# Performance work log

Measured on AMD Instinct MI355X. Metric: run time of the kernel, lower is better.

## Reference

```python
import jax, jax.numpy as jnp
import numpy as np

EPS = 1e-8  # F.cosine_similarity default eps


def setup_inputs() -> dict:
    key = jax.random.key(0)
    k1, = jax.random.split(key, 1)
    x = jax.random.normal(k1, (16384, 512), dtype=jnp.float32)
    w = jnp.float32(10.0)   # init_w parameter
    b = jnp.float32(-5.0)   # init_b parameter
    return {"x": x, "w": w, "b": b}


def reference(x, w, b):
    # x: [2N, D] interleaved (anchor, positive) embeddings
    anchor = x[0::2]    # [N, D]
    positive = x[1::2]  # [N, D]
    N = anchor.shape[0]

    # cosine similarity matrix: cos[i, j] = <pos_i, anc_j> / max(|pos_i||anc_j|, eps)
    # (normalize + GEMM instead of the O(N*D*N) broadcast)
    dots = jnp.einsum('id,jd->ij', positive, anchor)          # [N, N]
    pn = jnp.linalg.norm(positive, axis=1)                    # [N]
    an = jnp.linalg.norm(anchor, axis=1)                      # [N]
    denom = jnp.maximum(pn[:, None] * an[None, :], EPS)
    cos_sim = dots / denom

    logits = cos_sim * w + b                                  # [N, N]
    labels = jnp.arange(N)

    # CrossEntropyLoss (mean reduction)
    logp = jax.nn.log_softmax(logits, axis=1)
    nloss = -jnp.mean(logp[jnp.arange(N), labels])
    return nloss
```

## Files before the change

kernel.cpp:

```cpp
#include <hip/hip_runtime.h>
#include <hip/hip_bf16.h>

typedef __attribute__((ext_vector_type(8))) short short8;
typedef __attribute__((ext_vector_type(4))) float f32x4;

#define D 512
#define BM 64
#define BN 64
#define BK 64

__device__ inline unsigned pack2f(float lo, float hi) {
    __hip_bfloat162 v = __float22bfloat162_rn(make_float2(lo, hi));
    union { __hip_bfloat162 h; unsigned u; } cv;
    cv.h = v;
    return cv.u;
}

__device__ inline int4 pack8f(const float4& v0, const float4& v1, float sc) {
    int4 r;
    r.x = (int)pack2f(v0.x * sc, v0.y * sc);
    r.y = (int)pack2f(v0.z * sc, v0.w * sc);
    r.z = (int)pack2f(v1.x * sc, v1.y * sc);
    r.w = (int)pack2f(v1.z * sc, v1.w * sc);
    return r;
}

__global__ __launch_bounds__(256) void norm_kernel(
    const float* __restrict__ x,
    float* __restrict__ pinv, float* __restrict__ ainv,
    float* __restrict__ diag, float* __restrict__ sumexp,
    __hip_bfloat16* __restrict__ Pn, __hip_bfloat16* __restrict__ An, int cached)
{
    const int i = blockIdx.x, t = threadIdx.x;
    const float2* ap = (const float2*)(x + (size_t)(2 * i) * D);
    const float2* pp = (const float2*)(x + (size_t)(2 * i + 1) * D);
    float2 a = ap[t], p = pp[t];
    float ssa = a.x * a.x + a.y * a.y;
    float ssp = p.x * p.x + p.y * p.y;
    float dt  = p.x * a.x + p.y * a.y;
#pragma unroll
    for (int m = 1; m < 64; m <<= 1) {
        ssa += __shfl_xor(ssa, m);
        ssp += __shfl_xor(ssp, m);
        dt  += __shfl_xor(dt, m);
    }
    __shared__ float red[3][4];
    if ((t & 63) == 0) { int wv = t >> 6; red[0][wv] = ssa; red[1][wv] = ssp; red[2][wv] = dt; }
    __syncthreads();
    ssa = red[0][0] + red[0][1] + red[0][2] + red[0][3];
    ssp = red[1][0] + red[1][1] + red[1][2] + red[1][3];
    dt  = red[2][0] + red[2][1] + red[2][2] + red[2][3];
    float an = sqrtf(ssa), pn = sqrtf(ssp);
    float ia = 1.0f / fmaxf(an, 1e-30f);
    float ip = 1.0f / fmaxf(pn, 1e-30f);
    if (t == 0) {
        ainv[i] = ia;
        pinv[i] = ip;
        diag[i] = dt / fmaxf(pn * an, 1e-8f);
        sumexp[i] = 0.0f;
    }
    if (cached) {
        ((__hip_bfloat162*)(Pn + (size_t)i * D))[t] = __float22bfloat162_rn(make_float2(p.x * ip, p.y * ip));
        ((__hip_bfloat162*)(An + (size_t)i * D))[t] = __float22bfloat162_rn(make_float2(a.x * ia, a.y * ia));
    }
}

template<bool CACHED>
__global__ __launch_bounds__(256, 2) void gemm_lse_kernel(
    const float* __restrict__ x,
    const __hip_bfloat16* __restrict__ Pn, const __hip_bfloat16* __restrict__ An,
    const float* __restrict__ pinv, const float* __restrict__ ainv,
    const float* __restrict__ wp, float* __restrict__ sumexp, int N)
{
    __shared__ __align__(16) unsigned char lds[81920];
    unsigned char* As = lds;
    unsigned char* Bs = lds + 65536;

    const int t = threadIdx.x;
    const int rb = blockIdx.y, cs = blockIdx.x;
    const int lane = t & 63, w = t >> 6;
    const int wr = w >> 1, wc = w & 1;
    const int l15 = lane & 15, lhi = lane >> 4;

    const int colsPer = N >> 3;
    const int CT = colsPer / BN;
    const int Q = CT * (D / BK);

    {
        int r = t >> 2;
        int kq = (t & 3) << 7;
        int grow = rb * BM + r;
        if (CACHED) {
            const int4* src = (const int4*)(Pn + (size_t)grow * D);
#pragma unroll
            for (int i2 = 0; i2 < 16; ++i2) {
                int k0 = kq + i2 * 8;
                int4 v = src[k0 >> 3];
                *(int4*)(As + r * 1024 + ((k0 * 2) ^ ((r & 7) << 4))) = v;
            }
        } else {
            const float4* src = (const float4*)(x + (size_t)(2 * grow + 1) * D);
            float sc = pinv[grow];
#pragma unroll
            for (int i2 = 0; i2 < 16; ++i2) {
                int k0 = kq + i2 * 8;
                float4 v0 = src[k0 >> 2], v1 = src[(k0 >> 2) + 1];
                *(int4*)(As + r * 1024 + ((k0 * 2) ^ ((r & 7) << 4))) = pack8f(v0, v1, sc);
            }
        }
    }

    const int cl = t >> 2;
    const int kq = (t & 3) << 4;

    auto loadB = [&](int q, int4& oa, int4& ob) {
        int ct = q >> 3, kc = q & 7;
        int c = cs * colsPer + ct * BN + cl;
        int k = kc * BK + kq;
        if (CACHED) {
            const int4* src = (const int4*)(An + (size_t)c * D + k);
            oa = src[0]; ob = src[1];
        } else {
            const float4* src = (const float4*)(x + (size_t)(2 * c) * D + k);
            float sc = ainv[c];
            float4 v0 = src[0], v1 = src[1], v2 = src[2], v3 = src[3];
            oa = pack8f(v0, v1, sc);
            ob = pack8f(v2, v3, sc);
        }
    };
    auto writeB = [&](int buf, const int4& oa, const int4& ob) {
        unsigned char* bb = Bs + buf * 8192 + cl * 128;
        int kb0 = kq * 2;
        *(int4*)(bb + (kb0 ^ ((cl & 7) << 4))) = oa;
        *(int4*)(bb + ((kb0 + 16) ^ ((cl & 7) << 4))) = ob;
    };

    const float wv = *wp;
    const float s = fabsf(wv);

    int4 ba, bb2;
    loadB(0, ba, bb2);
    __syncthreads();
    writeB(0, ba, bb2);
    __syncthreads();

    f32x4 acc[2][2];
    float rs[2][4];
#pragma unroll
    for (int mi = 0; mi < 2; ++mi) {
#pragma unroll
        for (int j = 0; j < 4; ++j) rs[mi][j] = 0.0f;
#pragma unroll
        for (int ni = 0; ni < 2; ++ni) {
#pragma unroll
            for (int j = 0; j < 4; ++j) acc[mi][ni][j] = 0.0f;
        }
    }

    for (int q = 0; q < Q; ++q) {
        const int kc = q & 7;
        const bool more = (q + 1 < Q);
        if (more) loadB(q + 1, ba, bb2);
        const unsigned char* Bp = Bs + (q & 1) * 8192;
#pragma unroll
        for (int ks = 0; ks < 2; ++ks) {
            int ka = kc * 64 + ks * 32 + lhi * 8;
            int ra0 = wr * 32 + l15, ra1 = ra0 + 16;
            short8 a0 = *(const short8*)(As + ra0 * 1024 + ((ka * 2) ^ ((ra0 & 7) << 4)));
            short8 a1 = *(const short8*)(As + ra1 * 1024 + ((ka * 2) ^ ((ra1 & 7) << 4)));
            int kb = ks * 32 + lhi * 8;
            int c0 = wc * 32 + l15, c1 = c0 + 16;
            short8 b0 = *(const short8*)(Bp + c0 * 128 + ((kb * 2) ^ ((c0 & 7) << 4)));
            short8 b1 = *(const short8*)(Bp + c1 * 128 + ((kb * 2) ^ ((c1 & 7) << 4)));
            acc[0][0] = __builtin_amdgcn_mfma_f32_16x16x32_bf16(a0, b0, acc[0][0], 0, 0, 0);
            acc[0][1] = __builtin_amdgcn_mfma_f32_16x16x32_bf16(a0, b1, acc[0][1], 0, 0, 0);
            acc[1][0] = __builtin_amdgcn_mfma_f32_16x16x32_bf16(a1, b0, acc[1][0], 0, 0, 0);
            acc[1][1] = __builtin_amdgcn_mfma_f32_16x16x32_bf16(a1, b1, acc[1][1], 0, 0, 0);
        }
        if (kc == 7) {
#pragma unroll
            for (int mi = 0; mi < 2; ++mi) {
#pragma unroll
                for (int ni = 0; ni < 2; ++ni) {
#pragma unroll
                    for (int j = 0; j < 4; ++j) {
                        rs[mi][j] += __expf(acc[mi][ni][j] * wv - s);
                        acc[mi][ni][j] = 0.0f;
                    }
                }
            }
        }
        if (more) {
            __syncthreads();
            writeB((q + 1) & 1, ba, bb2);
            __syncthreads();
        }
    }

#pragma unroll
    for (int mi = 0; mi < 2; ++mi) {
#pragma unroll
        for (int j = 0; j < 4; ++j) {
            float v = rs[mi][j];
            v += __shfl_xor(v, 1);
            v += __shfl_xor(v, 2);
            v += __shfl_xor(v, 4);
            v += __shfl_xor(v, 8);
            if (l15 == 0) {
                int row = rb * BM + wr * 32 + mi * 16 + lhi * 4 + j;
                atomicAdd(&sumexp[row], v);
            }
        }
    }
}

__global__ __launch_bounds__(256) void finalize_kernel(
    const float* __restrict__ sumexp, const float* __restrict__ diag,
    const float* __restrict__ wp, float* __restrict__ out, int N)
{
    const int t = threadIdx.x;
    const float w = *wp;
    const float s = fabsf(w);
    float acc = 0.0f;
    for (int i = t; i < N; i += 256)
        acc += s + logf(sumexp[i]) - w * diag[i];
#pragma unroll
    for (int m = 1; m < 64; m <<= 1) acc += __shfl_xor(acc, m);
    __shared__ float red[4];
    if ((t & 63) == 0) red[t >> 6] = acc;
    __syncthreads();
    if (t == 0) out[0] = (red[0] + red[1] + red[2] + red[3]) / (float)N;
}

extern "C" void kernel_launch(void* const* d_in, const int* in_sizes, int n_in,
                              void* d_out, int out_size, void* d_ws, size_t ws_size,
                              hipStream_t stream) {
    const float* x  = (const float*)d_in[0];
    const float* wp = (const float*)d_in[1];

    const int N = in_sizes[0] / (2 * D);

    char* ws = (char*)d_ws;
    size_t nf = (size_t)N * 4;
    float* pinv   = (float*)(ws);
    float* ainv   = (float*)(ws + nf);
    float* diag   = (float*)(ws + 2 * nf);
    float* sumexp = (float*)(ws + 3 * nf);
    size_t base = (4 * nf + 255) & ~(size_t)255;
    __hip_bfloat16* Pn = (__hip_bfloat16*)(ws + base);
    __hip_bfloat16* An = (__hip_bfloat16*)(ws + base + (size_t)N * D * 2);
    const bool cached = ws_size >= base + (size_t)N * D * 4;

    norm_kernel<<<N, 256, 0, stream>>>(x, pinv, ainv, diag, sumexp, Pn, An, cached ? 1 : 0);

    dim3 grid(8, N / BM);
    if (cached)
        gemm_lse_kernel<true><<<grid, 256, 0, stream>>>(x, Pn, An, pinv, ainv, wp, sumexp, N);
    else
        gemm_lse_kernel<false><<<grid, 256, 0, stream>>>(x, Pn, An, pinv, ainv, wp, sumexp, N);

    finalize_kernel<<<1, 256, 0, stream>>>(sumexp, diag, wp, (float*)d_out, N);
}
```

Measured before the change: 218.5 us.

## Use 128x128 output tiles with direct global-to-LDS loads in cached GEMM path

Adds a new cached-path GEMM+LSE kernel that computes a full 128x128 output tile per block over a 2D grid. Each warp now holds 4x4 MFMA accumulators, and operands are streamed straight into LDS with global_load_lds. This replaces the old design, where a 64-row A panel stayed resident and each block swept a column slice. The aim is more MFMA work per LDS read and less per-tile load overhead. In exchange the tile loop is not double-buffered (load, sync, compute, sync), and atomics on sumexp increase because there are many column blocks. The finalize kernel is widened to 1024 threads.

```diff
diff --git a/kernel.cpp b/kernel.cpp
--- a/kernel.cpp
+++ b/kernel.cpp
@@ -5,9 +5,12 @@
 typedef __attribute__((ext_vector_type(4))) float f32x4;
 
 #define D 512
-#define BM 64
-#define BN 64
+#define BM 128
+#define BN 128
 #define BK 64
+
+typedef const __attribute__((address_space(1))) void gvoid;
+typedef __attribute__((address_space(3))) void lvoid;
 
 __device__ inline unsigned pack2f(float lo, float hi) {
     __hip_bfloat162 v = __float22bfloat162_rn(make_float2(lo, hi));
@@ -65,10 +68,92 @@
     }
 }
 
-template<bool CACHED>
-__global__ __launch_bounds__(256, 2) void gemm_lse_kernel(
+__global__ __launch_bounds__(256) void gemm_lse_128(
+    const __hip_bfloat16* __restrict__ Pn, const __hip_bfloat16* __restrict__ An,
+    const float* __restrict__ wp, float* __restrict__ sumexp)
+{
+    __shared__ __align__(16) unsigned char lds[32768];
+    unsigned char* As = lds;
+    unsigned char* Bs = lds + 16384;
+
+    const int t = threadIdx.x;
+    const int lane = t & 63, w = t >> 6;
+    const int wr = w >> 1, wc = w & 1;
+    const int l15 = lane & 15, lhi = lane >> 4;
+    const int brow = blockIdx.y * BM;
+    const int bcol = blockIdx.x * BN;
+
+    const float wv = *wp;
+    const float s = fabsf(wv);
+
+    f32x4 acc[4][4];
+#pragma unroll
+    for (int mi = 0; mi < 4; ++mi)
+#pragma unroll
+        for (int ni = 0; ni < 4; ++ni)
+#pragma unroll
+            for (int j = 0; j < 4; ++j) acc[mi][ni][j] = 0.0f;
+
+    const int o0 = t * 16;
+
+    for (int kt = 0; kt < D / BK; ++kt) {
+#pragma unroll
+        for (int i = 0; i < 4; ++i) {
+            int o = i * 4096 + o0;
+            int row = o >> 7;
+            int sslot = ((o >> 4) & 7) ^ (row & 7);
+            const __hip_bfloat16* ga = Pn + (size_t)(brow + row) * D + kt * BK + sslot * 8;
+            const __hip_bfloat16* gb = An + (size_t)(bcol + row) * D + kt * BK + sslot * 8;
+            __builtin_amdgcn_global_load_lds((gvoid*)ga, (lvoid*)(As + o), 16, 0, 0);
+            __builtin_amdgcn_global_load_lds((gvoid*)gb, (lvoid*)(Bs + o), 16, 0, 0);
+        }
+        __syncthreads();
+
+#pragma unroll
+        for (int ks = 0; ks < 2; ++ks) {
+            short8 a[4], b[4];
+            const int kb = ks * 64 + lhi * 16;
+#pragma unroll
+            for (int mi = 0; mi < 4; ++mi) {
+                int r = wr * 64 + mi * 16 + l15;
+                a[mi] = *(const short8*)(As + r * 128 + (kb ^ ((r & 7) << 4)));
+            }
+#pragma unroll
+            for (int ni = 0; ni < 4; ++ni) {
+                int c = wc * 64 + ni * 16 + l15;
+                b[ni] = *(const short8*)(Bs + c * 128 + (kb ^ ((c & 7) << 4)));
+            }
+#pragma unroll
+            for (int mi = 0; mi < 4; ++mi)
+#pragma unroll
+                for (int ni = 0; ni < 4; ++ni)
+                    acc[mi][ni] = __builtin_amdgcn_mfma_f32_16x16x32_bf16(a[mi], b[ni], acc[mi][ni], 0, 0, 0);
+        }
+        __syncthreads();
+    }
+
+#pragma unroll
+    for (int mi = 0; mi < 4; ++mi) {
+#pragma unroll
+        for (int j = 0; j < 4; ++j) {
+            float v = 0.0f;
+#pragma unroll
+            for (int ni = 0; ni < 4; ++ni)
+                v += __expf(acc[mi][ni][j] * wv - s);
+            v += __shfl_xor(v, 1);
+            v += __shfl_xor(v, 2);
+            v += __shfl_xor(v, 4);
+            v += __shfl_xor(v, 8);
+            if (l15 == 0) {
+                int row = brow + wr * 64 + mi * 16 + lhi * 4 + j;
+                atomicAdd(&sumexp[row], v);
+            }
+        }
+    }
+}
+
+__global__ __launch_bounds__(256, 2) void gemm_lse_small(
     const float* __restrict__ x,
-    const __hip_bfloat16* __restrict__ Pn, const __hip_bfloat16* __restrict__ An,
     const float* __restrict__ pinv, const float* __restrict__ ainv,
     const float* __restrict__ wp, float* __restrict__ sumexp, int N)
 {
@@ -83,30 +168,20 @@
     const int l15 = lane & 15, lhi = lane >> 4;
 
     const int colsPer = N >> 3;
-    const int CT = colsPer / BN;
-    const int Q = CT * (D / BK);
+    const int CT = colsPer / 64;
+    const int Q = CT * (D / 64);
 
     {
         int r = t >> 2;
         int kq = (t & 3) << 7;
-        int grow = rb * BM + r;
-        if (CACHED) {
-            const int4* src = (const int4*)(Pn + (size_t)grow * D);
-#pragma unroll
-            for (int i2 = 0; i2 < 16; ++i2) {
-                int k0 = kq + i2 * 8;
-                int4 v = src[k0 >> 3];
-                *(int4*)(As + r * 1024 + ((k0 * 2) ^ ((r & 7) << 4))) = v;
-            }
-        } else {
-            const float4* src = (const float4*)(x + (size_t)(2 * grow + 1) * D);
-            float sc = pinv[grow];
-#pragma unroll
-            for (int i2 = 0; i2 < 16; ++i2) {
-                int k0 = kq + i2 * 8;
-                float4 v0 = src[k0 >> 2], v1 = src[(k0 >> 2) + 1];
-                *(int4*)(As + r * 1024 + ((k0 * 2) ^ ((r & 7) << 4))) = pack8f(v0, v1, sc);
-            }
+        int grow = rb * 64 + r;
+        const float4* src = (const float4*)(x + (size_t)(2 * grow + 1) * D);
+        float sc = pinv[grow];
+#pragma unroll
+        for (int i2 = 0; i2 < 16; ++i2) {
+            int k0 = kq + i2 * 8;
+            float4 v0 = src[k0 >> 2], v1 = src[(k0 >> 2) + 1];
+            *(int4*)(As + r * 1024 + ((k0 * 2) ^ ((r & 7) << 4))) = pack8f(v0, v1, sc);
         }
     }
 
@@ -115,18 +190,13 @@
 
     auto loadB = [&](int q, int4& oa, int4& ob) {
         int ct = q >> 3, kc = q & 7;
-        int c = cs * colsPer + ct * BN + cl;
-        int k = kc * BK + kq;
-        if (CACHED) {
-            const int4* src = (const int4*)(An + (size_t)c * D + k);
-            oa = src[0]; ob = src[1];
-        } else {
-            const float4* src = (const float4*)(x + (size_t)(2 * c) * D + k);
-            float sc = ainv[c];
-            float4 v0 = src[0], v1 = src[1], v2 = src[2], v3 = src[3];
-            oa = pack8f(v0, v1, sc);
-            ob = pack8f(v2, v3, sc);
-        }
+        int c = cs * colsPer + ct * 64 + cl;
+        int k = kc * 64 + kq;
+        const float4* src = (const float4*)(x + (size_t)(2 * c) * D + k);
+        float sc = ainv[c];
+        float4 v0 = src[0], v1 = src[1], v2 = src[2], v3 = src[3];
+        oa = pack8f(v0, v1, sc);
+        ob = pack8f(v2, v3, sc);
     };
     auto writeB = [&](int buf, const int4& oa, const int4& ob) {
         unsigned char* bb = Bs + buf * 8192 + cl * 128;
@@ -151,10 +221,9 @@
 #pragma unroll
         for (int j = 0; j < 4; ++j) rs[mi][j] = 0.0f;
 #pragma unroll
-        for (int ni = 0; ni < 2; ++ni) {
+        for (int ni = 0; ni < 2; ++ni)
 #pragma unroll
             for (int j = 0; j < 4; ++j) acc[mi][ni][j] = 0.0f;
-        }
     }
 
     for (int q = 0; q < Q; ++q) {
@@ -179,16 +248,14 @@
         }
         if (kc == 7) {
 #pragma unroll
-            for (int mi = 0; mi < 2; ++mi) {
-#pragma unroll
-                for (int ni = 0; ni < 2; ++ni) {
+            for (int mi = 0; mi < 2; ++mi)
+#pragma unroll
+                for (int ni = 0; ni < 2; ++ni)
 #pragma unroll
                     for (int j = 0; j < 4; ++j) {
                         rs[mi][j] += __expf(acc[mi][ni][j] * wv - s);
                         acc[mi][ni][j] = 0.0f;
                     }
-                }
-            }
         }
         if (more) {
             __syncthreads();
@@ -198,7 +265,7 @@
     }
 
 #pragma unroll
-    for (int mi = 0; mi < 2; ++mi) {
+    for (int mi = 0; mi < 2; ++mi)
 #pragma unroll
         for (int j = 0; j < 4; ++j) {
             float v = rs[mi][j];
@@ -207,14 +274,13 @@
             v += __shfl_xor(v, 4);
             v += __shfl_xor(v, 8);
             if (l15 == 0) {
-                int row = rb * BM + wr * 32 + mi * 16 + lhi * 4 + j;
+                int row = rb * 64 + wr * 32 + mi * 16 + lhi * 4 + j;
                 atomicAdd(&sumexp[row], v);
             }
         }
-    }
-}
-
-__global__ __launch_bounds__(256) void finalize_kernel(
+}
+
+__global__ __launch_bounds__(1024) void finalize_kernel(
     const float* __restrict__ sumexp, const float* __restrict__ diag,
     const float* __restrict__ wp, float* __restrict__ out, int N)
 {
@@ -222,14 +288,19 @@
     const float w = *wp;
     const float s = fabsf(w);
     float acc = 0.0f;
-    for (int i = t; i < N; i += 256)
+    for (int i = t; i < N; i += 1024)
         acc += s + logf(sumexp[i]) - w * diag[i];
 #pragma unroll
     for (int m = 1; m < 64; m <<= 1) acc += __shfl_xor(acc, m);
-    __shared__ float red[4];
+    __shared__ float red[16];
     if ((t & 63) == 0) red[t >> 6] = acc;
     __syncthreads();
-    if (t == 0) out[0] = (red[0] + red[1] + red[2] + red[3]) / (float)N;
+    if (t == 0) {
+        float v = 0.0f;
+#pragma unroll
+        for (int i = 0; i < 16; ++i) v += red[i];
+        out[0] = v / (float)N;
+    }
 }
 
 extern "C" void kernel_launch(void* const* d_in, const int* in_sizes, int n_in,
@@ -253,11 +324,13 @@
 
     norm_kernel<<<N, 256, 0, stream>>>(x, pinv, ainv, diag, sumexp, Pn, An, cached ? 1 : 0);
 
-    dim3 grid(8, N / BM);
-    if (cached)
-        gemm_lse_kernel<true><<<grid, 256, 0, stream>>>(x, Pn, An, pinv, ainv, wp, sumexp, N);
-    else
-        gemm_lse_kernel<false><<<grid, 256, 0, stream>>>(x, Pn, An, pinv, ainv, wp, sumexp, N);
-
-    finalize_kernel<<<1, 256, 0, stream>>>(sumexp, diag, wp, (float*)d_out, N);
-}
+    if (cached) {
+        dim3 grid(N / BN, N / BM);
+        gemm_lse_128<<<grid, 256, 0, stream>>>(Pn, An, wp, sumexp);
+    } else {
+        dim3 grid(8, N / 64);
+        gemm_lse_small<<<grid, 256, 0, stream>>>(x, pinv, ainv, wp, sumexp, N);
+    }
+
+    finalize_kernel<<<1, 1024, 0, stream>>>(sumexp, diag, wp, (float*)d_out, N);
+}
```

Result: slower. 237.1 us (+8.5%).
